# Kernel tuning notes

Measured on AMD Instinct MI355X. Metric: run time of the kernel, lower is better.

The kernel has to match this reference:

```python
import jax, jax.numpy as jnp
import numpy as np

N, D, NUM_CLASSES = 4096, 512, 128
MARGIN = 0.3


def setup_inputs() -> dict:
    key = jax.random.key(0)
    k1, k2 = jax.random.split(key)
    embeddings = jax.random.normal(k1, (N, D), dtype=jnp.float32)
    labels = jax.random.randint(k2, (N,), 0, NUM_CLASSES, dtype=jnp.int64)
    return {"embeddings": embeddings, "labels": labels}


def _batch_hard_triplet(embeddings, labels, margin):
    # L2-normalize rows (torch F.normalize: x / max(||x||, eps))
    norm = jnp.linalg.norm(embeddings, axis=1, keepdims=True)
    e = embeddings / jnp.maximum(norm, 1e-12)
    n = e.shape[0]
    # Pairwise Euclidean distance via Gram matrix; ||a-b||^2 = 2 - 2 a.b for unit vectors
    gram = e @ e.T                                   # [N, N]
    sq = jnp.clip(2.0 - 2.0 * gram, 0.0, None)
    # safe sqrt: zero (and exactly-equal) pairs get distance 0 with zero gradient
    nz = sq > 0
    dist = jnp.where(nz, jnp.sqrt(jnp.where(nz, sq, 1.0)), 0.0)  # [N, N]

    same = labels[:, None] == labels[None, :]        # [N, N] bool
    eye = jnp.eye(n, dtype=bool)
    pos_mask = same & ~eye                           # positives excluding self
    neg_mask = ~same

    # hardest positive (row max over positives), hardest negative (row min over negatives)
    dist_ap = jnp.max(jnp.where(pos_mask, dist, -jnp.inf), axis=1)  # [N]
    dist_an = jnp.min(jnp.where(neg_mask, dist, jnp.inf), axis=1)   # [N]

    valid = jnp.any(pos_mask, axis=1) & jnp.any(neg_mask, axis=1)   # rows kept by torch loop
    per_row = jax.nn.relu(dist_ap - dist_an + margin)
    num_valid = jnp.sum(valid)
    loss_sum = jnp.sum(jnp.where(valid, per_row, 0.0))
    return jnp.where(num_valid > 0, loss_sum / jnp.maximum(num_valid, 1), 0.0)


def reference(embeddings, labels):
    return _batch_hard_triplet(embeddings, labels, MARGIN)
```

## Files before the change

### kernel.cpp

```cpp
#include <hip/hip_runtime.h>
#include <hip/hip_bf16.h>
#include <stdint.h>


#define NROW 4096
#define DIM  512
#define MARGIN 0.3f
#define BT 128
#define NTILE (NROW / BT)
#define NPAIR (NTILE * (NTILE + 1) / 2)
#define POS_INIT 0xFFFFFFFFu
#define NEG_INIT 0u

typedef __attribute__((ext_vector_type(8))) __bf16 bf16x8;
typedef __attribute__((ext_vector_type(4))) float  f32x4;
typedef __attribute__((ext_vector_type(8))) unsigned short u16x8;

__device__ __forceinline__ unsigned enc(float f) {
    unsigned u = __float_as_uint(f);
    return (u & 0x80000000u) ? ~u : (u | 0x80000000u);
}
__device__ __forceinline__ float dec(unsigned e) {
    return (e & 0x80000000u) ? __uint_as_float(e & 0x7fffffffu)
                             : __uint_as_float(~e);
}

__device__ __forceinline__ unsigned short f2bf(float f) {
    __hip_bfloat16 h = __float2bfloat16(f);
    return *reinterpret_cast<unsigned short*>(&h);
}

__global__ void tl_norm(const float* __restrict__ E,
                        __hip_bfloat16* __restrict__ Ebf,
                        unsigned* __restrict__ posArr,
                        unsigned* __restrict__ negArr) {
    if (blockIdx.x < 16) {
        int t = blockIdx.x * 256 + threadIdx.x;
        posArr[t] = POS_INIT;
        negArr[t] = NEG_INIT;
    }
    int wave = threadIdx.x >> 6;
    int lane = threadIdx.x & 63;
    int row  = blockIdx.x * 4 + wave;

    const float4* src = (const float4*)(E + (size_t)row * DIM);
    float4 v0 = src[2 * lane];
    float4 v1 = src[2 * lane + 1];
    float ss = v0.x*v0.x + v0.y*v0.y + v0.z*v0.z + v0.w*v0.w
             + v1.x*v1.x + v1.y*v1.y + v1.z*v1.z + v1.w*v1.w;
    #pragma unroll
    for (int m = 32; m >= 1; m >>= 1) ss += __shfl_xor(ss, m);
    float inv = 1.0f / fmaxf(sqrtf(ss), 1e-12f);

    u16x8 o;
    o[0] = f2bf(v0.x * inv); o[1] = f2bf(v0.y * inv);
    o[2] = f2bf(v0.z * inv); o[3] = f2bf(v0.w * inv);
    o[4] = f2bf(v1.x * inv); o[5] = f2bf(v1.y * inv);
    o[6] = f2bf(v1.z * inv); o[7] = f2bf(v1.w * inv);

    const int ktile = lane >> 2, c_in = lane & 3;
    const int rtile = row >> 4,  r_in = row & 15;
    const size_t off16 = (size_t)ktile * 16384 + (size_t)rtile * 64
                       + (size_t)c_in * 16 + r_in;
    ((u16x8*)Ebf)[off16] = o;
}

__global__ void __launch_bounds__(256, 2)
tl_gram(const __hip_bfloat16* __restrict__ Ebf,
        const int* __restrict__ labels,
        unsigned* __restrict__ posArr,
        unsigned* __restrict__ negArr) {
    __shared__ int rowLab[BT];
    __shared__ int colLab[BT];

    int bid = blockIdx.x;
    int t = (bid & 7) * (NPAIR / 8) + (bid >> 3);

    int bi = 0, rowlen = NTILE;
    while (t >= rowlen) { t -= rowlen; rowlen--; bi++; }
    const int bj = bi + t;

    const int tid  = threadIdx.x;
    const int wave = tid >> 6;
    const int lane = tid & 63;
    const int quad = lane >> 4;
    const int l16  = lane & 15;
    const int wr   = wave >> 1;
    const int wc   = wave & 1;
    const int tileI = bi * BT;
    const int tileJ = bj * BT;
    const bool diag = (bi == bj);

    if (tid < BT) rowLab[tid] = labels[tileI + tid];
    else          colLab[tid - BT] = labels[tileJ + (tid - BT)];
    __syncthreads();

    const bf16x8* Ev = (const bf16x8*)Ebf;
    const bf16x8* Ea = Ev + ((tileI + wr * 64) >> 4) * 64 + lane;
    const bf16x8* Eb = Ev + ((tileJ + wc * 64) >> 4) * 64 + lane;

    f32x4 acc[4][4] = {};
    bf16x8 a[4][4], b[4][4];

    #pragma unroll
    for (int p = 0; p < 3; ++p) {
        #pragma unroll
        for (int i = 0; i < 4; i++) {
            a[p][i] = Ea[p * 16384 + i * 64];
            b[p][i] = Eb[p * 16384 + i * 64];
        }
    }
    #pragma unroll
    for (int kk = 0; kk < 16; ++kk) {
        const int cur = kk & 3;
        if (kk + 3 < 16) {
            const int nxt = (kk + 3) & 3;
            #pragma unroll
            for (int i = 0; i < 4; i++) {
                a[nxt][i] = Ea[(kk + 3) * 16384 + i * 64];
                b[nxt][i] = Eb[(kk + 3) * 16384 + i * 64];
            }
        }
        #pragma unroll
        for (int mi = 0; mi < 4; mi++)
            #pragma unroll
            for (int ni = 0; ni < 4; ni++)
                acc[mi][ni] = __builtin_amdgcn_mfma_f32_16x16x32_bf16(
                    a[cur][mi], b[cur][ni], acc[mi][ni], 0, 0, 0);
    }

    int rl[16], cl[4], clocv[4];
    #pragma unroll
    for (int mi = 0; mi < 4; mi++)
        #pragma unroll
        for (int reg = 0; reg < 4; reg++)
            rl[mi * 4 + reg] = rowLab[wr * 64 + mi * 16 + quad * 4 + reg];
    #pragma unroll
    for (int ni = 0; ni < 4; ni++) {
        clocv[ni] = wc * 64 + ni * 16 + l16;
        cl[ni] = colLab[clocv[ni]];
    }

    #pragma unroll
    for (int mi = 0; mi < 4; mi++) {
        #pragma unroll
        for (int reg = 0; reg < 4; reg++) {
            const int rloc = wr * 64 + mi * 16 + quad * 4 + reg;
            const int lr   = rl[mi * 4 + reg];
            const int gi   = tileI + rloc;
            float pmin =  INFINITY;
            float nmax = -INFINITY;
            #pragma unroll
            for (int ni = 0; ni < 4; ni++) {
                const int gj  = tileJ + clocv[ni];
                const float g = acc[mi][ni][reg];
                const bool same = (lr == cl[ni]);
                if (same && gi != gj) pmin = fminf(pmin, g);
                if (!same)            nmax = fmaxf(nmax, g);
            }
            #pragma unroll
            for (int m = 1; m < 16; m <<= 1) {
                pmin = fminf(pmin, __shfl_xor(pmin, m));
                nmax = fmaxf(nmax, __shfl_xor(nmax, m));
            }
            if (l16 == 0) {
                if (pmin <  INFINITY) atomicMin(&posArr[gi], enc(pmin));
                if (nmax > -INFINITY) atomicMax(&negArr[gi], enc(nmax));
            }
        }
    }

    if (!diag) {
        #pragma unroll
        for (int ni = 0; ni < 4; ni++) {
            const int lc = cl[ni];
            const int gj = tileJ + clocv[ni];
            float pmin =  INFINITY;
            float nmax = -INFINITY;
            #pragma unroll
            for (int mi = 0; mi < 4; mi++) {
                #pragma unroll
                for (int reg = 0; reg < 4; reg++) {
                    const float g = acc[mi][ni][reg];
                    const bool same = (rl[mi * 4 + reg] == lc);
                    if (same) pmin = fminf(pmin, g);
                    else      nmax = fmaxf(nmax, g);
                }
            }
            pmin = fminf(pmin, __shfl_xor(pmin, 16));
            pmin = fminf(pmin, __shfl_xor(pmin, 32));
            nmax = fmaxf(nmax, __shfl_xor(nmax, 16));
            nmax = fmaxf(nmax, __shfl_xor(nmax, 32));
            if (quad == 0) {
                if (pmin <  INFINITY) atomicMin(&posArr[gj], enc(pmin));
                if (nmax > -INFINITY) atomicMax(&negArr[gj], enc(nmax));
            }
        }
    }
}

__global__ void tl_final(const unsigned* __restrict__ posArr,
                         const unsigned* __restrict__ negArr,
                         float* __restrict__ out) {
    const int tid = threadIdx.x;
    uint4 pe4 = ((const uint4*)posArr)[tid];
    uint4 ne4 = ((const uint4*)negArr)[tid];
    unsigned pes[4] = {pe4.x, pe4.y, pe4.z, pe4.w};
    unsigned nes[4] = {ne4.x, ne4.y, ne4.z, ne4.w};
    float sum = 0.0f;
    int   count = 0;
    #pragma unroll
    for (int j = 0; j < 4; j++) {
        const bool valid = (pes[j] != POS_INIT) && (nes[j] != NEG_INIT);
        const float dap = sqrtf(fmaxf(2.0f - 2.0f * dec(pes[j]), 0.0f));
        const float dan = sqrtf(fmaxf(2.0f - 2.0f * dec(nes[j]), 0.0f));
        const float per = fmaxf(dap - dan + MARGIN, 0.0f);
        if (valid) { sum += per; count += 1; }
    }
    #pragma unroll
    for (int m = 32; m >= 1; m >>= 1) {
        sum   += __shfl_xor(sum, m);
        count += __shfl_xor(count, m);
    }
    __shared__ float ssum[16];
    __shared__ int   scnt[16];
    const int wave = tid >> 6, lane = tid & 63;
    if (lane == 0) { ssum[wave] = sum; scnt[wave] = count; }
    __syncthreads();
    if (tid == 0) {
        float s = 0.0f; int c = 0;
        #pragma unroll
        for (int w = 0; w < 16; w++) { s += ssum[w]; c += scnt[w]; }
        out[0] = (c > 0) ? (s / (float)c) : 0.0f;
    }
}

extern "C" void kernel_launch(void* const* d_in, const int* in_sizes, int n_in,
                              void* d_out, int out_size, void* d_ws, size_t ws_size,
                              hipStream_t stream) {
    const float* E      = (const float*)d_in[0];
    const int*   labels = (const int*)d_in[1];
    float*       out    = (float*)d_out;

    char* ws = (char*)d_ws;
    __hip_bfloat16* Ebf   = (__hip_bfloat16*)ws;
    unsigned* posArr      = (unsigned*)(ws + (size_t)NROW * DIM * 2);
    unsigned* negArr      = posArr + NROW;

    tl_norm<<<NROW / 4, 256, 0, stream>>>(E, Ebf, posArr, negArr);
    tl_gram<<<NPAIR, 256, 0, stream>>>(Ebf, labels, posArr, negArr);
    tl_final<<<1, 1024, 0, stream>>>(posArr, negArr, out);
}
```

Measured before the change: 88.68 us.

## Fuse final reduction into gram kernel and split gram work across eight waves

The separate final-reduction kernel is dropped. The last gram block to finish, detected through an atomic done-counter, now computes the loss, which removes one kernel launch. The gram kernel uses 512 threads with 8 waves, each owning a 64x32 sub-tile. This halves per-wave accumulator and register use to raise occupancy, and the kernel uses a 3-stage register prefetch and s_setprio around the MFMAs. The norm kernel is restructured so each thread writes 4 contiguous 16-byte chunks per row. The cost is an extra atomic and threadfence in every block, plus more redundant label and A-fragment loads per block.

```diff
diff --git a/kernel.cpp b/kernel.cpp
--- a/kernel.cpp
+++ b/kernel.cpp
@@ -33,43 +33,56 @@
 __global__ void tl_norm(const float* __restrict__ E,
                         __hip_bfloat16* __restrict__ Ebf,
                         unsigned* __restrict__ posArr,
-                        unsigned* __restrict__ negArr) {
+                        unsigned* __restrict__ negArr,
+                        unsigned* __restrict__ doneCnt) {
     if (blockIdx.x < 16) {
         int t = blockIdx.x * 256 + threadIdx.x;
         posArr[t] = POS_INIT;
         negArr[t] = NEG_INIT;
     }
-    int wave = threadIdx.x >> 6;
-    int lane = threadIdx.x & 63;
-    int row  = blockIdx.x * 4 + wave;
-
-    const float4* src = (const float4*)(E + (size_t)row * DIM);
-    float4 v0 = src[2 * lane];
-    float4 v1 = src[2 * lane + 1];
-    float ss = v0.x*v0.x + v0.y*v0.y + v0.z*v0.z + v0.w*v0.w
-             + v1.x*v1.x + v1.y*v1.y + v1.z*v1.z + v1.w*v1.w;
-    #pragma unroll
-    for (int m = 32; m >= 1; m >>= 1) ss += __shfl_xor(ss, m);
-    float inv = 1.0f / fmaxf(sqrtf(ss), 1e-12f);
-
-    u16x8 o;
-    o[0] = f2bf(v0.x * inv); o[1] = f2bf(v0.y * inv);
-    o[2] = f2bf(v0.z * inv); o[3] = f2bf(v0.w * inv);
-    o[4] = f2bf(v1.x * inv); o[5] = f2bf(v1.y * inv);
-    o[6] = f2bf(v1.z * inv); o[7] = f2bf(v1.w * inv);
-
-    const int ktile = lane >> 2, c_in = lane & 3;
-    const int rtile = row >> 4,  r_in = row & 15;
-    const size_t off16 = (size_t)ktile * 16384 + (size_t)rtile * 64
-                       + (size_t)c_in * 16 + r_in;
-    ((u16x8*)Ebf)[off16] = o;
-}
-
-__global__ void __launch_bounds__(256, 2)
+    if (blockIdx.x == 16 && threadIdx.x == 0) *doneCnt = 0;
+
+    const int wave  = threadIdx.x >> 6;
+    const int lane  = threadIdx.x & 63;
+    const int r2    = lane >> 4;
+    const int kc    = lane & 15;
+    const int rtile = blockIdx.x;
+    const int r_in  = wave * 4 + r2;
+    const int row   = rtile * 16 + r_in;
+
+    const float4* src = (const float4*)(E + (size_t)row * DIM) + kc * 8;
+    float4 v[8];
+    #pragma unroll
+    for (int i = 0; i < 8; i++) v[i] = src[i];
+
+    float ss = 0.0f;
+    #pragma unroll
+    for (int i = 0; i < 8; i++)
+        ss += v[i].x*v[i].x + v[i].y*v[i].y + v[i].z*v[i].z + v[i].w*v[i].w;
+    #pragma unroll
+    for (int m = 1; m < 16; m <<= 1) ss += __shfl_xor(ss, m);
+    const float inv = 1.0f / fmaxf(sqrtf(ss), 1e-12f);
+
+    u16x8* dst = (u16x8*)Ebf + (size_t)kc * 16384 + (size_t)rtile * 64 + r_in;
+    #pragma unroll
+    for (int c = 0; c < 4; c++) {
+        const float4 lo = v[2*c], hi = v[2*c + 1];
+        u16x8 o;
+        o[0] = f2bf(lo.x * inv); o[1] = f2bf(lo.y * inv);
+        o[2] = f2bf(lo.z * inv); o[3] = f2bf(lo.w * inv);
+        o[4] = f2bf(hi.x * inv); o[5] = f2bf(hi.y * inv);
+        o[6] = f2bf(hi.z * inv); o[7] = f2bf(hi.w * inv);
+        dst[c * 16] = o;
+    }
+}
+
+__global__ void __launch_bounds__(512, 4)
 tl_gram(const __hip_bfloat16* __restrict__ Ebf,
         const int* __restrict__ labels,
         unsigned* __restrict__ posArr,
-        unsigned* __restrict__ negArr) {
+        unsigned* __restrict__ negArr,
+        unsigned* __restrict__ doneCnt,
+        float* __restrict__ out) {
     __shared__ int rowLab[BT];
     __shared__ int colLab[BT];
 
@@ -85,59 +98,61 @@
     const int lane = tid & 63;
     const int quad = lane >> 4;
     const int l16  = lane & 15;
-    const int wr   = wave >> 1;
-    const int wc   = wave & 1;
+    const int wr   = wave >> 2;
+    const int wc   = wave & 3;
     const int tileI = bi * BT;
     const int tileJ = bj * BT;
     const bool diag = (bi == bj);
 
-    if (tid < BT) rowLab[tid] = labels[tileI + tid];
-    else          colLab[tid - BT] = labels[tileJ + (tid - BT)];
+    if (tid < BT)            rowLab[tid] = labels[tileI + tid];
+    else if (tid < 2 * BT)   colLab[tid - BT] = labels[tileJ + (tid - BT)];
     __syncthreads();
 
     const bf16x8* Ev = (const bf16x8*)Ebf;
     const bf16x8* Ea = Ev + ((tileI + wr * 64) >> 4) * 64 + lane;
-    const bf16x8* Eb = Ev + ((tileJ + wc * 64) >> 4) * 64 + lane;
-
-    f32x4 acc[4][4] = {};
-    bf16x8 a[4][4], b[4][4];
-
-    #pragma unroll
-    for (int p = 0; p < 3; ++p) {
-        #pragma unroll
-        for (int i = 0; i < 4; i++) {
-            a[p][i] = Ea[p * 16384 + i * 64];
-            b[p][i] = Eb[p * 16384 + i * 64];
-        }
+    const bf16x8* Eb = Ev + ((tileJ + wc * 32) >> 4) * 64 + lane;
+
+    f32x4 acc[4][2] = {};
+    bf16x8 a[3][4], b[3][2];
+
+    #pragma unroll
+    for (int p = 0; p < 2; ++p) {
+        #pragma unroll
+        for (int mi = 0; mi < 4; mi++) a[p][mi] = Ea[p * 16384 + mi * 64];
+        #pragma unroll
+        for (int ni = 0; ni < 2; ni++) b[p][ni] = Eb[p * 16384 + ni * 64];
     }
     #pragma unroll
     for (int kk = 0; kk < 16; ++kk) {
-        const int cur = kk & 3;
-        if (kk + 3 < 16) {
-            const int nxt = (kk + 3) & 3;
-            #pragma unroll
-            for (int i = 0; i < 4; i++) {
-                a[nxt][i] = Ea[(kk + 3) * 16384 + i * 64];
-                b[nxt][i] = Eb[(kk + 3) * 16384 + i * 64];
-            }
-        }
+        const int cur = kk % 3;
+        if (kk + 2 < 16) {
+            const int nx = (kk + 2) % 3;
+            #pragma unroll
+            for (int mi = 0; mi < 4; mi++)
+                a[nx][mi] = Ea[(kk + 2) * 16384 + mi * 64];
+            #pragma unroll
+            for (int ni = 0; ni < 2; ni++)
+                b[nx][ni] = Eb[(kk + 2) * 16384 + ni * 64];
+        }
+        __builtin_amdgcn_s_setprio(1);
         #pragma unroll
         for (int mi = 0; mi < 4; mi++)
             #pragma unroll
-            for (int ni = 0; ni < 4; ni++)
+            for (int ni = 0; ni < 2; ni++)
                 acc[mi][ni] = __builtin_amdgcn_mfma_f32_16x16x32_bf16(
                     a[cur][mi], b[cur][ni], acc[mi][ni], 0, 0, 0);
-    }
-
-    int rl[16], cl[4], clocv[4];
+        __builtin_amdgcn_s_setprio(0);
+    }
+
+    int rl[16], cl[2], clocv[2];
     #pragma unroll
     for (int mi = 0; mi < 4; mi++)
         #pragma unroll
         for (int reg = 0; reg < 4; reg++)
             rl[mi * 4 + reg] = rowLab[wr * 64 + mi * 16 + quad * 4 + reg];
     #pragma unroll
-    for (int ni = 0; ni < 4; ni++) {
-        clocv[ni] = wc * 64 + ni * 16 + l16;
+    for (int ni = 0; ni < 2; ni++) {
+        clocv[ni] = wc * 32 + ni * 16 + l16;
         cl[ni] = colLab[clocv[ni]];
     }
 
@@ -151,7 +166,7 @@
             float pmin =  INFINITY;
             float nmax = -INFINITY;
             #pragma unroll
-            for (int ni = 0; ni < 4; ni++) {
+            for (int ni = 0; ni < 2; ni++) {
                 const int gj  = tileJ + clocv[ni];
                 const float g = acc[mi][ni][reg];
                 const bool same = (lr == cl[ni]);
@@ -172,7 +187,7 @@
 
     if (!diag) {
         #pragma unroll
-        for (int ni = 0; ni < 4; ni++) {
+        for (int ni = 0; ni < 2; ni++) {
             const int lc = cl[ni];
             const int gj = tileJ + clocv[ni];
             float pmin =  INFINITY;
@@ -197,41 +212,42 @@
             }
         }
     }
-}
-
-__global__ void tl_final(const unsigned* __restrict__ posArr,
-                         const unsigned* __restrict__ negArr,
-                         float* __restrict__ out) {
-    const int tid = threadIdx.x;
-    uint4 pe4 = ((const uint4*)posArr)[tid];
-    uint4 ne4 = ((const uint4*)negArr)[tid];
-    unsigned pes[4] = {pe4.x, pe4.y, pe4.z, pe4.w};
-    unsigned nes[4] = {ne4.x, ne4.y, ne4.z, ne4.w};
-    float sum = 0.0f;
-    int   count = 0;
-    #pragma unroll
-    for (int j = 0; j < 4; j++) {
-        const bool valid = (pes[j] != POS_INIT) && (nes[j] != NEG_INIT);
-        const float dap = sqrtf(fmaxf(2.0f - 2.0f * dec(pes[j]), 0.0f));
-        const float dan = sqrtf(fmaxf(2.0f - 2.0f * dec(nes[j]), 0.0f));
-        const float per = fmaxf(dap - dan + MARGIN, 0.0f);
-        if (valid) { sum += per; count += 1; }
-    }
-    #pragma unroll
-    for (int m = 32; m >= 1; m >>= 1) {
-        sum   += __shfl_xor(sum, m);
-        count += __shfl_xor(count, m);
-    }
-    __shared__ float ssum[16];
-    __shared__ int   scnt[16];
-    const int wave = tid >> 6, lane = tid & 63;
-    if (lane == 0) { ssum[wave] = sum; scnt[wave] = count; }
+
+    __shared__ unsigned sOld;
+    __threadfence();
     __syncthreads();
-    if (tid == 0) {
-        float s = 0.0f; int c = 0;
-        #pragma unroll
-        for (int w = 0; w < 16; w++) { s += ssum[w]; c += scnt[w]; }
-        out[0] = (c > 0) ? (s / (float)c) : 0.0f;
+    if (tid == 0) sOld = atomicAdd(doneCnt, 1u);
+    __syncthreads();
+    if (sOld == NPAIR - 1) {
+        __threadfence();
+        float sum = 0.0f;
+        int   cnt = 0;
+        for (int i = tid; i < NROW; i += 512) {
+            const unsigned pe = __hip_atomic_load(&posArr[i], __ATOMIC_RELAXED,
+                                                  __HIP_MEMORY_SCOPE_AGENT);
+            const unsigned ne = __hip_atomic_load(&negArr[i], __ATOMIC_RELAXED,
+                                                  __HIP_MEMORY_SCOPE_AGENT);
+            const bool valid = (pe != POS_INIT) && (ne != NEG_INIT);
+            const float dap = sqrtf(fmaxf(2.0f - 2.0f * dec(pe), 0.0f));
+            const float dan = sqrtf(fmaxf(2.0f - 2.0f * dec(ne), 0.0f));
+            const float per = fmaxf(dap - dan + MARGIN, 0.0f);
+            if (valid) { sum += per; cnt += 1; }
+        }
+        #pragma unroll
+        for (int m = 32; m >= 1; m >>= 1) {
+            sum += __shfl_xor(sum, m);
+            cnt += __shfl_xor(cnt, m);
+        }
+        __shared__ float ssum[8];
+        __shared__ int   scnt[8];
+        if (lane == 0) { ssum[wave] = sum; scnt[wave] = cnt; }
+        __syncthreads();
+        if (tid == 0) {
+            float s = 0.0f; int c = 0;
+            #pragma unroll
+            for (int w = 0; w < 8; w++) { s += ssum[w]; c += scnt[w]; }
+            out[0] = (c > 0) ? (s / (float)c) : 0.0f;
+        }
     }
 }
 
@@ -246,8 +262,8 @@
     __hip_bfloat16* Ebf   = (__hip_bfloat16*)ws;
     unsigned* posArr      = (unsigned*)(ws + (size_t)NROW * DIM * 2);
     unsigned* negArr      = posArr + NROW;
-
-    tl_norm<<<NROW / 4, 256, 0, stream>>>(E, Ebf, posArr, negArr);
-    tl_gram<<<NPAIR, 256, 0, stream>>>(Ebf, labels, posArr, negArr);
-    tl_final<<<1, 1024, 0, stream>>>(posArr, negArr, out);
-}
+    unsigned* doneCnt     = negArr + NROW;
+
+    tl_norm<<<NROW / 16, 256, 0, stream>>>(E, Ebf, posArr, negArr, doneCnt);
+    tl_gram<<<NPAIR, 512, 0, stream>>>(Ebf, labels, posArr, negArr, doneCnt, out);
+}
```

Result: slower. 187.1 us (+111.0%).
